# Kernel optimization log

Measured on AMD Instinct MI355X. Metric: run time of the kernel, lower is better.

The kernel has to match this reference:

```python
import jax, jax.numpy as jnp
import numpy as np

B, N, RESC, LAT, UNIT = 8, 32, 256.0, 1536, 512
CHS = [64, 64, 128, 256, 512, 512]
HS = [128, 64, 32, 16, 8, 1]


def _align(feat, P):
    # torch F.grid_sample(feat, 2*P.unsqueeze(-2)/RESC - 1, 'bilinear', 'border', align_corners=False).squeeze(-1)
    # feat: [B,C,H,W], P: [B,M,2] (x,y) pixel coords in [0,RESC); returns [B,C,M]
    Bn, C, H, W = feat.shape
    gx = 2.0 * P[..., 0] / RESC - 1.0
    gy = 2.0 * P[..., 1] / RESC - 1.0
    # align_corners=False unnormalize, then border clamp
    x = jnp.clip(((gx + 1.0) * W - 1.0) * 0.5, 0.0, W - 1.0)
    y = jnp.clip(((gy + 1.0) * H - 1.0) * 0.5, 0.0, H - 1.0)
    x0 = jnp.floor(x); y0 = jnp.floor(y)
    wx = (x - x0)[:, None, :]; wy = (y - y0)[:, None, :]
    x0i = x0.astype(jnp.int32); y0i = y0.astype(jnp.int32)
    x1i = jnp.minimum(x0i + 1, W - 1); y1i = jnp.minimum(y0i + 1, H - 1)
    flat = feat.reshape(Bn, C, H * W)
    def gat(yi, xi):
        return jnp.take_along_axis(flat, (yi * W + xi)[:, None, :], axis=2)  # [B,C,M]
    v00 = gat(y0i, x0i); v01 = gat(y0i, x1i); v10 = gat(y1i, x0i); v11 = gat(y1i, x1i)
    return v00 * (1 - wx) * (1 - wy) + v01 * wx * (1 - wy) + v10 * (1 - wx) * wy + v11 * wx * wy


def _conv1(x, w, b):
    # 1x1 Conv1d: [B,Cin,M] x [Cout,Cin] -> [B,Cout,M]
    return jnp.einsum('bci,oc->boi', x, w) + b[None, :, None]


def _rescls(x, p):
    # ResCls(n=1): intro -> (relu(BN) -> chorus, residual) -> outro ; BN in eval mode
    iw, ib, bg, bb, bm, bv, cw, cb, ow, ob = p
    x = _conv1(x, iw, ib)
    d = jax.nn.relu((x - bm[None, :, None]) * (bg / jnp.sqrt(bv + 1e-5))[None, :, None] + bb[None, :, None])
    x = x + _conv1(d, cw, cb)
    return _conv1(x, ow, ob)


def _forward(feats, P, n, gp, pp):
    # node features: concat of per-level aligned features  [B, LAT, N]
    F_ = jnp.concatenate([_align(f, P) for f in feats], axis=1)
    # edge midpoints ep[b, i*N+j] = (P[i] + P[j]) / 2  -> [B, N*N, 2]
    ep = ((P[:, :, None, :] + P[:, None, :, :]) * 0.5).reshape(B, N * N, 2)
    # L: first LAT channels = F[:, :, i], next LAT channels = F[:, :, j]
    Fi = jnp.broadcast_to(F_[:, :, :, None], (B, LAT, N, N)).reshape(B, LAT, N * N)
    Fj = jnp.broadcast_to(F_[:, :, None, :], (B, LAT, N, N)).reshape(B, LAT, N * N)
    E = jnp.concatenate([_align(f, ep) for f in feats], axis=1)  # [B, LAT, N*N]
    CE = jnp.concatenate([Fi, Fj, E], axis=1)  # [B, 3*LAT, N*N]
    gate = jax.nn.sigmoid(_rescls(CE, gp))  # [B, 1, N*N]
    pr = _rescls(CE, pp)  # [B, 64, N*N]
    pr = pr / jnp.maximum(jnp.linalg.norm(pr, axis=1, keepdims=True), 1e-12)  # F.normalize(dim=1)
    m = jnp.arange(N) < n[:, None]  # [B, N]
    mask = (m[:, None, :] & m[:, :, None]).reshape(B, 1, N * N).astype(CE.dtype)
    return (gate * pr * mask).reshape(B, 64, N, N)


def setup_inputs() -> dict:
    key = jax.random.key(0)
    ks = jax.random.split(key, 20)
    d = {}
    for i, (c, h) in enumerate(zip(CHS, HS)):
        d[f'feat{i}'] = jax.random.normal(ks[i], (B, c, h, h), jnp.float32)
    d['P'] = jax.random.uniform(ks[6], (B, N, 2), jnp.float32) * RESC
    d['n'] = jax.random.randint(ks[7], (B,), 16, N + 1, jnp.int32)
    def w(k, shape):
        return jax.random.normal(k, shape, jnp.float32) * 0.02
    for pre, cout, k0 in (('g', 1, 8), ('p', 64, 12)):
        d[pre + '_iw'] = w(ks[k0], (UNIT, 3 * LAT)); d[pre + '_ib'] = jnp.zeros((UNIT,), jnp.float32)
        d[pre + '_bg'] = jnp.ones((UNIT,), jnp.float32); d[pre + '_bb'] = jnp.zeros((UNIT,), jnp.float32)
        d[pre + '_bm'] = jnp.zeros((UNIT,), jnp.float32)
        d[pre + '_bv'] = jax.random.uniform(ks[k0 + 1], (UNIT,), jnp.float32) + 0.5
        d[pre + '_cw'] = w(ks[k0 + 2], (UNIT, UNIT)); d[pre + '_cb'] = jnp.zeros((UNIT,), jnp.float32)
        d[pre + '_ow'] = w(ks[k0 + 3], (cout, UNIT)); d[pre + '_ob'] = jnp.zeros((cout,), jnp.float32)
    return d


def reference(feat0, feat1, feat2, feat3, feat4, feat5, P, n,
              g_iw, g_ib, g_bg, g_bb, g_bm, g_bv, g_cw, g_cb, g_ow, g_ob,
              p_iw, p_ib, p_bg, p_bb, p_bm, p_bv, p_cw, p_cb, p_ow, p_ob):
    feats = (feat0, feat1, feat2, feat3, feat4, feat5)
    gp = (g_iw, g_ib, g_bg, g_bb, g_bm, g_bv, g_cw, g_cb, g_ow, g_ob)
    pp = (p_iw, p_ib, p_bg, p_bb, p_bm, p_bv, p_cw, p_cb, p_ow, p_ob)
    return _forward(feats, P, n, gp, pp)
```

## Files before the change

kernel.cpp:

```cpp
#include <hip/hip_runtime.h>
#include <hip/hip_bf16.h>

using bf16 = __hip_bfloat16;
using short8 = __attribute__((ext_vector_type(8))) short;
using f32x4  = __attribute__((ext_vector_type(4))) float;
typedef unsigned int u32;

#define LAT_ 1536

__device__ __forceinline__ void glds16(const bf16* g, bf16* l) {
  __builtin_amdgcn_global_load_lds(
      (const __attribute__((address_space(1))) void*)g,
      (__attribute__((address_space(3))) void*)l, 16, 0, 0);
}
__device__ __forceinline__ float b2f(bf16 x) { return __bfloat162float(x); }
__device__ __forceinline__ bf16 f2b(float x) { return __float2bfloat16(x); }

template<int C, int W>
__device__ __forceinline__ void trans_tile(const float* __restrict__ src, bf16* __restrict__ dst,
                                           int b, int hw0, int c0, bf16 (*tile)[72], int t) {
  constexpr int HW = W * W;
  {
    int cl = t >> 2, h0 = (t & 3) * 16;
    const float* sp = src + (long)(b * C + c0 + cl) * HW + hw0 + h0;
    #pragma unroll
    for (int k = 0; k < 16; k += 4) {
      float4 v = *(const float4*)(sp + k);
      tile[h0 + k + 0][cl] = f2b(v.x);
      tile[h0 + k + 1][cl] = f2b(v.y);
      tile[h0 + k + 2][cl] = f2b(v.z);
      tile[h0 + k + 3][cl] = f2b(v.w);
    }
  }
  __syncthreads();
  {
    int hwl = t >> 2, cc = (t & 3) * 16;
    bf16* dp = dst + ((long)b * HW + hw0 + hwl) * C + c0 + cc;
    #pragma unroll
    for (int k = 0; k < 16; k += 2) {
      __hip_bfloat162 pr;
      pr.x = tile[hwl][cc + k];
      pr.y = tile[hwl][cc + k + 1];
      *(__hip_bfloat162*)(dp + k) = pr;
    }
  }
}

__global__ __launch_bounds__(256) void prep_k(
    const float* __restrict__ g_iw, const float* __restrict__ p_iw,
    const float* __restrict__ p_cw, const float* __restrict__ p_ow, const float* __restrict__ f5,
    const float* __restrict__ g_bg, const float* __restrict__ g_bb, const float* __restrict__ g_bm,
    const float* __restrict__ g_bv, const float* __restrict__ p_bg, const float* __restrict__ p_bb,
    const float* __restrict__ p_bm, const float* __restrict__ p_bv,
    const float* __restrict__ g_ib, const float* __restrict__ p_ib, const float* __restrict__ p_cb,
    const float* __restrict__ g_ow, const float* __restrict__ g_cw,
    const float* __restrict__ g_cb, const float* __restrict__ g_ob,
    const float* __restrict__ f0, const float* __restrict__ f1, const float* __restrict__ f2,
    const float* __restrict__ f3, const float* __restrict__ f4,
    bf16* __restrict__ Wp, bf16* __restrict__ pcw16, bf16* __restrict__ pow16,
    bf16* __restrict__ T5, float* __restrict__ bnp, float* __restrict__ u,
    float* __restrict__ gacc,
    bf16* __restrict__ T0, bf16* __restrict__ T1, bf16* __restrict__ T2,
    bf16* __restrict__ T3, bf16* __restrict__ T4) {
  __shared__ bf16 tile[64][72];
  __shared__ float red[256];
  int B = blockIdx.x, t = threadIdx.x;
  if (B < 18432) {
    int seg = B / 3072;
    int idx = (B % 3072) * 256 + t;
    if (idx < 512 * 1536) {
      int r = idx / 1536, c = idx % 1536;
      const float* src; int co;
      switch (seg) {
        case 0: src = g_iw; co = 0;    break;
        case 1: src = g_iw; co = 1536; break;
        case 2: src = p_iw; co = 0;    break;
        case 3: src = p_iw; co = 1536; break;
        case 4: src = g_iw; co = 3072; break;
        default: src = p_iw; co = 3072; break;
      }
      Wp[(long)seg * 512 * 1536 + idx] = f2b(src[(long)r * 4608 + co + c]);
    }
    return;
  }
  if (B < 19456) { int idx = (B - 18432) * 256 + t; pcw16[idx] = f2b(p_cw[idx]); return; }
  if (B < 19584) { int idx = (B - 19456) * 256 + t; pow16[idx] = f2b(p_ow[idx]); return; }
  if (B < 19600) { int idx = (B - 19584) * 256 + t; T5[idx] = f2b(f5[idx]); return; }
  if (B < 19602) {
    int k = (B - 19600) * 256 + t;
    if (k < 512) {
      float sg = g_bg[k] / sqrtf(g_bv[k] + 1e-5f);
      bnp[k] = sg; bnp[512 + k] = g_bb[k] - g_bm[k] * sg;
      float sp = p_bg[k] / sqrtf(p_bv[k] + 1e-5f);
      bnp[1024 + k] = sp; bnp[1536 + k] = p_bb[k] - p_bm[k] * sp;
      bnp[2048 + k] = g_ib[k]; bnp[2560 + k] = p_ib[k];
      bnp[3584 + k] = p_cb[k];
    }
    return;
  }
  if (B < 19610) {
    __shared__ float ured[4][64];
    int k0 = (B - 19602) * 64;
    int kk = t & 63, part = t >> 6;
    int k = k0 + kk;
    float s = 0.f;
    for (int o = part * 128; o < part * 128 + 128; ++o)
      s = fmaf(g_ow[o], g_cw[o * 512 + k], s);
    ured[part][kk] = s;
    __syncthreads();
    if (part == 0) u[k] = ured[0][kk] + ured[1][kk] + ured[2][kk] + ured[3][kk];
    return;
  }
  if (B == 19610) {
    red[t] = g_ow[t] * g_cb[t] + g_ow[t + 256] * g_cb[t + 256];
    __syncthreads();
    for (int off = 128; off; off >>= 1) {
      if (t < off) red[t] += red[t + off];
      __syncthreads();
    }
    if (t == 0) bnp[3072] = red[0] + g_ob[0];
    return;
  }
  if (B < 19643) { int idx = (B - 19611) * 256 + t; gacc[idx] = 0.f; return; }
  {
    int q = B - 19643;
    int b = q / 376, tt = q % 376;
    if (tt < 256)      trans_tile<64, 128>(f0, T0, b, tt * 64, 0, tile, t);
    else if (tt < 320) trans_tile<64, 64 >(f1, T1, b, (tt - 256) * 64, 0, tile, t);
    else if (tt < 352) { int z = tt - 320; trans_tile<128, 32>(f2, T2, b, (z & 15) * 64, (z >> 4) * 64, tile, t); }
    else if (tt < 368) { int z = tt - 352; trans_tile<256, 16>(f3, T3, b, (z & 3) * 64, (z >> 2) * 64, tile, t); }
    else               { int z = tt - 368; trans_tile<512, 8 >(f4, T4, b, 0, z * 64, tile, t); }
  }
}

__device__ __forceinline__ float blo(u32 r) { return __uint_as_float(r << 16); }
__device__ __forceinline__ float bhi(u32 r) { return __uint_as_float(r & 0xffff0000u); }

template<int C, int W>
__device__ __forceinline__ void proc2(const bf16* __restrict__ T, int b,
    const float* MX, const float* MY, bf16* __restrict__ Sb, int koff, int t) {
  constexpr int C2 = C / 2, HW = W * W;
  const bf16* Tb = T + (long)b * HW * C;
  for (int idx = t; idx < 16 * C2; idx += 256) {
    int q = idx / C2, c2 = idx % C2;
    float x = MX[q], y = MY[q];
    float fx = fminf(fmaxf(x * ((float)W / 256.f) - 0.5f, 0.f), (float)(W - 1));
    float fy = fminf(fmaxf(y * ((float)W / 256.f) - 0.5f, 0.f), (float)(W - 1));
    float x0f = floorf(fx), y0f = floorf(fy);
    float wx = fx - x0f, wy = fy - y0f;
    int x0 = (int)x0f, y0 = (int)y0f;
    int x1 = min(x0 + 1, W - 1), y1 = min(y0 + 1, W - 1);
    u32 r00 = *(const u32*)&Tb[(y0 * W + x0) * C + 2 * c2];
    u32 r01 = *(const u32*)&Tb[(y0 * W + x1) * C + 2 * c2];
    u32 r10 = *(const u32*)&Tb[(y1 * W + x0) * C + 2 * c2];
    u32 r11 = *(const u32*)&Tb[(y1 * W + x1) * C + 2 * c2];
    float w00 = (1.f - wx) * (1.f - wy), w01 = wx * (1.f - wy);
    float w10 = (1.f - wx) * wy,        w11 = wx * wy;
    float vlo = blo(r00) * w00 + blo(r01) * w01 + blo(r10) * w10 + blo(r11) * w11;
    float vhi = bhi(r00) * w00 + bhi(r01) * w01 + bhi(r10) * w10 + bhi(r11) * w11;
    __hip_bfloat162 pr;
    pr.x = f2b(vlo); pr.y = f2b(vhi);
    *(__hip_bfloat162*)&Sb[(long)q * LAT_ + koff + 2 * c2] = pr;
  }
}

__global__ __launch_bounds__(256) void sample5_k(
    const bf16* __restrict__ T0, const bf16* __restrict__ T1, const bf16* __restrict__ T2,
    const bf16* __restrict__ T3, const bf16* __restrict__ T4, const bf16* __restrict__ T5,
    const float* __restrict__ P, bf16* __restrict__ Sball) {
  int b = blockIdx.z, p0 = blockIdx.x * 16, lvl = blockIdx.y, t = threadIdx.x;
  __shared__ float Px[32], Py[32], MX[16], MY[16];
  if (t < 32) { Px[t] = P[(b * 32 + t) * 2]; Py[t] = P[(b * 32 + t) * 2 + 1]; }
  __syncthreads();
  if (t < 16) {
    int m = p0 + t;
    float x, y;
    if (m < 32) { x = Px[m]; y = Py[m]; }
    else { int ij = m - 32, i = ij >> 5, j = ij & 31;
           x = 0.5f * (Px[i] + Px[j]); y = 0.5f * (Py[i] + Py[j]); }
    MX[t] = x; MY[t] = y;
  }
  __syncthreads();
  bf16* Sb = Sball + ((long)b * 1056 + p0) * LAT_;
  switch (lvl) {
    case 0: proc2<64, 128>(T0, b, MX, MY, Sb, 0,    t); break;
    case 1: proc2<64, 64 >(T1, b, MX, MY, Sb, 64,   t); break;
    case 2: proc2<128, 32>(T2, b, MX, MY, Sb, 128,  t); break;
    case 3: proc2<256, 16>(T3, b, MX, MY, Sb, 256,  t); break;
    case 4: proc2<512, 8 >(T4, b, MX, MY, Sb, 512,  t); break;
    default:
      for (int idx = t; idx < 16 * 256; idx += 256) {
        int q = idx >> 8, c2 = idx & 255;
        *(__hip_bfloat162*)&Sb[(long)q * LAT_ + 1024 + 2 * c2] =
            *(const __hip_bfloat162*)&T5[b * 512 + 2 * c2];
      }
  }
}

__global__ __launch_bounds__(256) void nodegemm_k(
    const bf16* __restrict__ Sball, const bf16* __restrict__ Wp, float* __restrict__ A4) {
  int b = blockIdx.y;
  int n0 = blockIdx.x * 64;
  int t = threadIdx.x, w = t >> 6, lane = t & 63;
  int nn = n0 + w * 16;
  int frow = lane & 15, fko = (lane >> 4) * 8;
  const bf16* Ab = Sball + (long)b * 1056 * LAT_;
  f32x4 acc[2] = {};
  for (int kb = 0; kb < LAT_; kb += 32) {
    short8 bq = *(const short8*)&Wp[(long)(nn + frow) * LAT_ + kb + fko];
    #pragma unroll
    for (int i = 0; i < 2; ++i) {
      short8 aq = *(const short8*)&Ab[(long)(i * 16 + frow) * LAT_ + kb + fko];
      acc[i] = __builtin_amdgcn_mfma_f32_16x16x32_bf16(aq, bq, acc[i], 0, 0, 0);
    }
  }
  #pragma unroll
  for (int i = 0; i < 2; ++i)
    #pragma unroll
    for (int r = 0; r < 4; ++r) {
      int m = i * 16 + (lane >> 4) * 4 + r;
      int n = nn + (lane & 15);
      A4[(long)b * 65536 + m * 2048 + n] = acc[i][r];
    }
}

__global__ __launch_bounds__(256) void edge_k(
    const bf16* __restrict__ Sball, const bf16* __restrict__ WpE,
    const float* __restrict__ bnp, const float* __restrict__ A4,
    const float* __restrict__ u, const float* __restrict__ g_ow,
    bf16* __restrict__ XFh, bf16* __restrict__ DH, float* __restrict__ gacc) {
  int b = blockIdx.z;
  int m0 = blockIdx.x * 128, n0 = blockIdx.y * 128;
  const bf16* A = Sball + (long)b * 1056 * LAT_ + 32 * LAT_;
  __shared__ bf16 Ash[128 * 64];
  __shared__ bf16 Bsh[128 * 64];
  int t = threadIdx.x, w = t >> 6, lane = t & 63;
  int mh = (w & 1) * 64, nh = (w >> 1) * 64;
  int frow = lane & 15, kq = lane >> 4;
  int srow = w * 8 + (lane >> 3), schunk = lane & 7;
  int rx7 = frow & 7;
  f32x4 acc[4][4] = {};
  for (int kb = 0; kb < LAT_; kb += 64) {
    #pragma unroll
    for (int q = 0; q < 4; ++q) {
      int ra = q * 32 + srow;
      int sc = (schunk ^ (ra & 7)) * 8;
      glds16(&A[(long)(m0 + ra) * LAT_ + kb + sc],   &Ash[ra * 64 + schunk * 8]);
      glds16(&WpE[(long)(n0 + ra) * LAT_ + kb + sc], &Bsh[ra * 64 + schunk * 8]);
    }
    __syncthreads();
    #pragma unroll
    for (int h = 0; h < 2; ++h) {
      int s8 = (((h * 4 + kq) ^ rx7) << 3);
      short8 af[4], bq[4];
      #pragma unroll
      for (int i = 0; i < 4; ++i)
        af[i] = *(const short8*)&Ash[(mh + i * 16 + frow) * 64 + s8];
      #pragma unroll
      for (int j = 0; j < 4; ++j)
        bq[j] = *(const short8*)&Bsh[(nh + j * 16 + frow) * 64 + s8];
      #pragma unroll
      for (int i = 0; i < 4; ++i)
        #pragma unroll
        for (int j = 0; j < 4; ++j)
          acc[i][j] = __builtin_amdgcn_mfma_f32_16x16x32_bf16(af[i], bq[j], acc[i][j], 0, 0, 0);
    }
    __syncthreads();
  }
  if (n0 < 512) {
    float pg[16];
    #pragma unroll
    for (int z = 0; z < 16; ++z) pg[z] = 0.f;
    #pragma unroll
    for (int i = 0; i < 4; ++i) {
      #pragma unroll
      for (int j = 0; j < 4; ++j) {
        int n = n0 + nh + j * 16 + (lane & 15);
        float gw = g_ow[n], uu = u[n];
        float sc2 = bnp[n], sh = bnp[512 + n], ib = bnp[2048 + n];
        #pragma unroll
        for (int r = 0; r < 4; ++r) {
          int m = m0 + mh + i * 16 + (lane >> 4) * 4 + r;
          float v = acc[i][j][r] + ib
                  + A4[((long)b * 32 + (m >> 5)) * 2048 + n]
                  + A4[((long)b * 32 + (m & 31)) * 2048 + 512 + n];
          float d = fmaxf(fmaf(v, sc2, sh), 0.f);
          pg[i * 4 + r] += gw * v + uu * d;
        }
      }
    }
    #pragma unroll
    for (int z = 0; z < 16; ++z) {
      float v = pg[z];
      v += __shfl_xor(v, 1, 16);
      v += __shfl_xor(v, 2, 16);
      v += __shfl_xor(v, 4, 16);
      v += __shfl_xor(v, 8, 16);
      pg[z] = v;
    }
    if ((lane & 15) == 0) {
      #pragma unroll
      for (int z = 0; z < 16; ++z) {
        int m = m0 + mh + (z >> 2) * 16 + (lane >> 4) * 4 + (z & 3);
        atomicAdd(&gacc[(long)b * 1024 + m], pg[z]);
      }
    }
  } else {
    #pragma unroll
    for (int i = 0; i < 4; ++i) {
      #pragma unroll
      for (int j = 0; j < 4; ++j) {
        int n = n0 + nh + j * 16 + (lane & 15);
        int np = n - 512;
        float sc2 = bnp[1024 + np], sh = bnp[1536 + np], ib = bnp[2048 + n];
        #pragma unroll
        for (int r = 0; r < 4; ++r) {
          int m = m0 + mh + i * 16 + (lane >> 4) * 4 + r;
          float v = acc[i][j][r] + ib
                  + A4[((long)b * 32 + (m >> 5)) * 2048 + 1024 + np]
                  + A4[((long)b * 32 + (m & 31)) * 2048 + 1536 + np];
          long e = ((long)b * 1024 + m) * 512 + np;
          XFh[e] = f2b(v);
          DH[e]  = f2b(fmaxf(fmaf(v, sc2, sh), 0.f));
        }
      }
    }
  }
}

__global__ __launch_bounds__(256) void chorus_k(
    const bf16* __restrict__ DH, const bf16* __restrict__ pcw16,
    const float* __restrict__ bnp, const bf16* __restrict__ XFh,
    bf16* __restrict__ Yp16) {
  int b = blockIdx.z;
  int m0 = blockIdx.x * 128, n0 = blockIdx.y * 128;
  const bf16* A = DH + (long)b * 1024 * 512;
  __shared__ bf16 Ash[128 * 64];
  __shared__ bf16 Bsh[128 * 64];
  int t = threadIdx.x, w = t >> 6, lane = t & 63;
  int mh = (w & 1) * 64, nh = (w >> 1) * 64;
  int frow = lane & 15, kq = lane >> 4;
  int srow = w * 8 + (lane >> 3), schunk = lane & 7;
  int rx7 = frow & 7;
  f32x4 acc[4][4] = {};
  for (int kb = 0; kb < 512; kb += 64) {
    #pragma unroll
    for (int q = 0; q < 4; ++q) {
      int ra = q * 32 + srow;
      int sc = (schunk ^ (ra & 7)) * 8;
      glds16(&A[(long)(m0 + ra) * 512 + kb + sc],     &Ash[ra * 64 + schunk * 8]);
      glds16(&pcw16[(long)(n0 + ra) * 512 + kb + sc], &Bsh[ra * 64 + schunk * 8]);
    }
    __syncthreads();
    #pragma unroll
    for (int h = 0; h < 2; ++h) {
      int s8 = (((h * 4 + kq) ^ rx7) << 3);
      short8 af[4], bq[4];
      #pragma unroll
      for (int i = 0; i < 4; ++i)
        af[i] = *(const short8*)&Ash[(mh + i * 16 + frow) * 64 + s8];
      #pragma unroll
      for (int j = 0; j < 4; ++j)
        bq[j] = *(const short8*)&Bsh[(nh + j * 16 + frow) * 64 + s8];
      #pragma unroll
      for (int i = 0; i < 4; ++i)
        #pragma unroll
        for (int j = 0; j < 4; ++j)
          acc[i][j] = __builtin_amdgcn_mfma_f32_16x16x32_bf16(af[i], bq[j], acc[i][j], 0, 0, 0);
    }
    __syncthreads();
  }
  #pragma unroll
  for (int i = 0; i < 4; ++i)
    #pragma unroll
    for (int j = 0; j < 4; ++j)
      #pragma unroll
      for (int r = 0; r < 4; ++r) {
        int m = m0 + mh + i * 16 + (lane >> 4) * 4 + r;
        int n = n0 + nh + j * 16 + (lane & 15);
        float v = acc[i][j][r] + bnp[3584 + n]
                + b2f(XFh[((long)b * 1024 + m) * 512 + n]);
        Yp16[((long)b * 1024 + m) * 512 + n] = f2b(v);
      }
}

__global__ __launch_bounds__(256) void ofinal_k(
    const bf16* __restrict__ Yp16, const bf16* __restrict__ pow16,
    const float* __restrict__ p_ob, const float* __restrict__ gacc,
    const float* __restrict__ bnp, const int* __restrict__ nvec,
    float* __restrict__ out) {
  int b = blockIdx.y;
  int m0 = blockIdx.x * 64;
  const bf16* Ab = Yp16 + (long)b * 1024 * 512;
  __shared__ bf16 Ash[64][40];
  __shared__ bf16 Bsh[64][40];
  __shared__ float ol[64][65];
  int t = threadIdx.x, w = t >> 6, lane = t & 63;
  int mq = w * 16;
  int frow = lane & 15, fko = (lane >> 4) * 8;
  f32x4 acc[4] = {};
  for (int kb = 0; kb < 512; kb += 32) {
    { int r = t >> 2, ko = (t & 3) * 8;
      *(uint4*)&Ash[r][ko] = *(const uint4*)&Ab[(long)(m0 + r) * 512 + kb + ko];
      *(uint4*)&Bsh[r][ko] = *(const uint4*)&pow16[(long)r * 512 + kb + ko]; }
    __syncthreads();
    short8 af = *(const short8*)&Ash[mq + frow][fko];
    #pragma unroll
    for (int j = 0; j < 4; ++j) {
      short8 bq = *(const short8*)&Bsh[j * 16 + frow][fko];
      acc[j] = __builtin_amdgcn_mfma_f32_16x16x32_bf16(af, bq, acc[j], 0, 0, 0);
    }
    __syncthreads();
  }
  float pr[4][4], ssl[4] = {0.f, 0.f, 0.f, 0.f};
  #pragma unroll
  for (int j = 0; j < 4; ++j) {
    float bias = p_ob[j * 16 + (lane & 15)];
    #pragma unroll
    for (int r = 0; r < 4; ++r) {
      float v = acc[j][r] + bias;
      pr[j][r] = v;
      ssl[r] = fmaf(v, v, ssl[r]);
    }
  }
  #pragma unroll
  for (int r = 0; r < 4; ++r) {
    float v = ssl[r];
    v += __shfl_xor(v, 1, 16);
    v += __shfl_xor(v, 2, 16);
    v += __shfl_xor(v, 4, 16);
    v += __shfl_xor(v, 8, 16);
    ssl[r] = v;
  }
  int nb = nvec[b];
  float gconst = bnp[3072];
  float scale[4];
  #pragma unroll
  for (int r = 0; r < 4; ++r) {
    int m = m0 + mq + (lane >> 4) * 4 + r;
    float gl = gacc[(long)b * 1024 + m] + gconst;
    float gate = 1.f / (1.f + expf(-gl));
    int ii = m >> 5, jj = m & 31;
    float maskv = (ii < nb && jj < nb) ? 1.f : 0.f;
    scale[r] = gate * maskv / fmaxf(sqrtf(ssl[r]), 1e-12f);
  }
  #pragma unroll
  for (int j = 0; j < 4; ++j)
    #pragma unroll
    for (int r = 0; r < 4; ++r)
      ol[mq + (lane >> 4) * 4 + r][j * 16 + (lane & 15)] = pr[j][r] * scale[r];
  __syncthreads();
  {
    int c = t >> 2, ms = (t & 3) * 16;
    float* op = out + ((long)b * 64 + c) * 1024 + m0 + ms;
    #pragma unroll
    for (int k = 0; k < 16; k += 4) {
      float4 v;
      v.x = ol[ms + k + 0][c];
      v.y = ol[ms + k + 1][c];
      v.z = ol[ms + k + 2][c];
      v.w = ol[ms + k + 3][c];
      *(float4*)(op + k) = v;
    }
  }
}

extern "C" void kernel_launch(void* const* d_in, const int* in_sizes, int n_in,
                              void* d_out, int out_size, void* d_ws, size_t ws_size,
                              hipStream_t stream) {
  const float* f0 = (const float*)d_in[0];
  const float* f1 = (const float*)d_in[1];
  const float* f2 = (const float*)d_in[2];
  const float* f3 = (const float*)d_in[3];
  const float* f4 = (const float*)d_in[4];
  const float* f5 = (const float*)d_in[5];
  const float* P  = (const float*)d_in[6];
  const int*   n  = (const int*)d_in[7];
  const float *g_iw=(const float*)d_in[8],  *g_ib=(const float*)d_in[9],
              *g_bg=(const float*)d_in[10], *g_bb=(const float*)d_in[11],
              *g_bm=(const float*)d_in[12], *g_bv=(const float*)d_in[13],
              *g_cw=(const float*)d_in[14], *g_cb=(const float*)d_in[15],
              *g_ow=(const float*)d_in[16], *g_ob=(const float*)d_in[17];
  const float *p_iw=(const float*)d_in[18], *p_ib=(const float*)d_in[19],
              *p_bg=(const float*)d_in[20], *p_bb=(const float*)d_in[21],
              *p_bm=(const float*)d_in[22], *p_bv=(const float*)d_in[23],
              *p_cw=(const float*)d_in[24], *p_cb=(const float*)d_in[25],
              *p_ow=(const float*)d_in[26], *p_ob=(const float*)d_in[27];
  float* out = (float*)d_out;
  char* wsb = (char*)d_ws;

  bf16*  Sb    = (bf16*)(wsb + 0);
  bf16*  Wp    = (bf16*)(wsb + 25952256);
  bf16*  pcw16 = (bf16*)(wsb + 35389440);
  bf16*  pow16 = (bf16*)(wsb + 35913728);
  bf16*  T5    = (bf16*)(wsb + 35979264);
  float* bnp   = (float*)(wsb + 35987456);
  float* u     = (float*)(wsb + 36003840);
  float* gacc  = (float*)(wsb + 36005888);
  float* A4    = (float*)(wsb + 36038656);
  bf16*  XFh   = (bf16*)(wsb + 38135808);
  bf16*  DH    = (bf16*)(wsb + 46524416);
  bf16*  Yp16  = (bf16*)(wsb + 54913024);
  bf16*  T0 = (bf16*)(wsb + 38135808);
  bf16*  T1 = (bf16*)(wsb + 54913024);
  bf16*  T2 = (bf16*)(wsb + 59107328);
  bf16*  T3 = (bf16*)(wsb + 61204480);
  bf16*  T4 = (bf16*)(wsb + 62253056);
  bf16*  WpE = Wp + (long)2048 * LAT_;

  prep_k<<<22651, 256, 0, stream>>>(g_iw, p_iw, p_cw, p_ow, f5,
      g_bg, g_bb, g_bm, g_bv, p_bg, p_bb, p_bm, p_bv, g_ib, p_ib, p_cb,
      g_ow, g_cw, g_cb, g_ob, f0, f1, f2, f3, f4,
      Wp, pcw16, pow16, T5, bnp, u, gacc, T0, T1, T2, T3, T4);
  sample5_k<<<dim3(66, 6, 8), 256, 0, stream>>>(T0, T1, T2, T3, T4, T5, P, Sb);
  nodegemm_k<<<dim3(32, 8), 256, 0, stream>>>(Sb, Wp, A4);
  edge_k<<<dim3(8, 8, 8), 256, 0, stream>>>(Sb, WpE, bnp, A4, u, g_ow, XFh, DH, gacc);
  chorus_k<<<dim3(8, 4, 8), 256, 0, stream>>>(DH, pcw16, bnp, XFh, Yp16);
  ofinal_k<<<dim3(16, 8), 256, 0, stream>>>(Yp16, pow16, p_ob, gacc, bnp, n, out);
}
```

Baseline: 249.7 us.

## Double-buffer edge GEMM LDS tiles with async global-to-LDS prefetch

The edge_k GEMM main loop now uses two LDS buffers per operand and issues the global_load_lds for tile kt+2 while MFMAs run on the current tile. Fragments are read into registers first, then a barrier frees the buffer for the next prefetch, with explicit vmcnt waits and sched barriers controlling ordering. s_setprio is raised around the MFMA block. This aims to hide global load latency, at the cost of doubling LDS use (64KB per block), which may lower occupancy.

```diff
diff --git a/kernel.cpp b/kernel.cpp
--- a/kernel.cpp
+++ b/kernel.cpp
@@ -232,40 +232,68 @@
   int b = blockIdx.z;
   int m0 = blockIdx.x * 128, n0 = blockIdx.y * 128;
   const bf16* A = Sball + (long)b * 1056 * LAT_ + 32 * LAT_;
-  __shared__ bf16 Ash[128 * 64];
-  __shared__ bf16 Bsh[128 * 64];
+  __shared__ bf16 Ash[2][128 * 64];
+  __shared__ bf16 Bsh[2][128 * 64];
   int t = threadIdx.x, w = t >> 6, lane = t & 63;
   int mh = (w & 1) * 64, nh = (w >> 1) * 64;
   int frow = lane & 15, kq = lane >> 4;
   int srow = w * 8 + (lane >> 3), schunk = lane & 7;
   int rx7 = frow & 7;
   f32x4 acc[4][4] = {};
-  for (int kb = 0; kb < LAT_; kb += 64) {
+
+  auto STAGE = [&](int buf, int kt) {
+    int kb = kt * 64;
     #pragma unroll
     for (int q = 0; q < 4; ++q) {
       int ra = q * 32 + srow;
       int sc = (schunk ^ (ra & 7)) * 8;
-      glds16(&A[(long)(m0 + ra) * LAT_ + kb + sc],   &Ash[ra * 64 + schunk * 8]);
-      glds16(&WpE[(long)(n0 + ra) * LAT_ + kb + sc], &Bsh[ra * 64 + schunk * 8]);
-    }
-    __syncthreads();
+      glds16(&A[(long)(m0 + ra) * LAT_ + kb + sc],   &Ash[buf][ra * 64 + schunk * 8]);
+      glds16(&WpE[(long)(n0 + ra) * LAT_ + kb + sc], &Bsh[buf][ra * 64 + schunk * 8]);
+    }
+  };
+
+  STAGE(0, 0);
+  STAGE(1, 1);
+  asm volatile("s_waitcnt vmcnt(8)" ::: "memory");
+  __builtin_amdgcn_sched_barrier(0);
+  __builtin_amdgcn_s_barrier();
+  #pragma unroll 1
+  for (int kt = 0; kt < 24; ++kt) {
+    int c = kt & 1;
+    short8 af[2][4], bq[2][4];
     #pragma unroll
     for (int h = 0; h < 2; ++h) {
       int s8 = (((h * 4 + kq) ^ rx7) << 3);
-      short8 af[4], bq[4];
       #pragma unroll
       for (int i = 0; i < 4; ++i)
-        af[i] = *(const short8*)&Ash[(mh + i * 16 + frow) * 64 + s8];
+        af[h][i] = *(const short8*)&Ash[c][(mh + i * 16 + frow) * 64 + s8];
       #pragma unroll
       for (int j = 0; j < 4; ++j)
-        bq[j] = *(const short8*)&Bsh[(nh + j * 16 + frow) * 64 + s8];
+        bq[h][j] = *(const short8*)&Bsh[c][(nh + j * 16 + frow) * 64 + s8];
+    }
+    asm volatile("s_waitcnt lgkmcnt(0)" ::: "memory");
+    __builtin_amdgcn_sched_barrier(0);
+    __builtin_amdgcn_s_barrier();
+    if (kt + 2 < 24) STAGE(c, kt + 2);
+    __builtin_amdgcn_sched_barrier(0);
+    __builtin_amdgcn_s_setprio(1);
+    #pragma unroll
+    for (int h = 0; h < 2; ++h)
       #pragma unroll
       for (int i = 0; i < 4; ++i)
         #pragma unroll
         for (int j = 0; j < 4; ++j)
-          acc[i][j] = __builtin_amdgcn_mfma_f32_16x16x32_bf16(af[i], bq[j], acc[i][j], 0, 0, 0);
-    }
-    __syncthreads();
+          acc[i][j] = __builtin_amdgcn_mfma_f32_16x16x32_bf16(af[h][i], bq[h][j], acc[i][j], 0, 0, 0);
+    __builtin_amdgcn_s_setprio(0);
+    if (kt < 23) {
+      if (kt + 2 < 24) {
+        asm volatile("s_waitcnt vmcnt(8)" ::: "memory");
+      } else {
+        asm volatile("s_waitcnt vmcnt(0)" ::: "memory");
+      }
+      __builtin_amdgcn_sched_barrier(0);
+      __builtin_amdgcn_s_barrier();
+    }
   }
   if (n0 < 512) {
     float pg[16];
```

Result: no change. 248.3 us (-0.6%).
